# Optimization experiments

Hardware: AMD Instinct MI355X
Metric: run time of the kernel (lower is better)

Reference implementation:

```python
import jax, jax.numpy as jnp
import numpy as np

B, S, IN, H, T, OUT = 128, 336, 64, 1024, 96, 1


def _lstm_step(h, c, x, W_ih, W_hh, b_ih, b_hh):
    # PyTorch LSTM cell: gates in (i, f, g, o) order
    g = x @ W_ih.T + b_ih + h @ W_hh.T + b_hh  # [B, 4H]
    i, f, gg, o = jnp.split(g, 4, axis=-1)
    c_new = jax.nn.sigmoid(f) * c + jax.nn.sigmoid(i) * jnp.tanh(gg)
    h_new = jax.nn.sigmoid(o) * jnp.tanh(c_new)
    return h_new, c_new


def setup_inputs() -> dict:
    key = jax.random.key(0)
    ks = jax.random.split(key, 12)
    s = 0.05
    return {
        "src": jax.random.normal(ks[0], (B, S, IN), jnp.float32),
        "enc_W_ih": jax.random.normal(ks[1], (4 * H, IN), jnp.float32) * s,
        "enc_W_hh": jax.random.normal(ks[2], (4 * H, H), jnp.float32) * s,
        "enc_b_ih": jax.random.normal(ks[3], (4 * H,), jnp.float32) * s,
        "enc_b_hh": jax.random.normal(ks[4], (4 * H,), jnp.float32) * s,
        "dec_W_ih": jax.random.normal(ks[5], (4 * H, OUT + H), jnp.float32) * s,
        "dec_W_hh": jax.random.normal(ks[6], (4 * H, H), jnp.float32) * s,
        "dec_b_ih": jax.random.normal(ks[7], (4 * H,), jnp.float32) * s,
        "dec_b_hh": jax.random.normal(ks[8], (4 * H,), jnp.float32) * s,
        "attn_W": jax.random.normal(ks[9], (H, H), jnp.float32) * s,
        "fc_W": jax.random.normal(ks[10], (OUT, H), jnp.float32) * s,
        "fc_b": jax.random.normal(ks[11], (OUT,), jnp.float32) * s,
        "target_len": T,
    }


def reference(src, enc_W_ih, enc_W_hh, enc_b_ih, enc_b_hh,
              dec_W_ih, dec_W_hh, dec_b_ih, dec_b_hh,
              attn_W, fc_W, fc_b, target_len):
    batch = src.shape[0]
    hdim = enc_W_hh.shape[1]

    # ---- Encoder: single-layer LSTM over src, batch_first ----
    def enc_step(carry, x_t):
        h, c = carry
        h, c = _lstm_step(h, c, x_t, enc_W_ih, enc_W_hh, enc_b_ih, enc_b_hh)
        return (h, c), h

    h0 = jnp.zeros((batch, hdim), src.dtype)
    c0 = jnp.zeros((batch, hdim), src.dtype)
    (h_enc, c_enc), enc_hs = jax.lax.scan(enc_step, (h0, c0),
                                          jnp.swapaxes(src, 0, 1))
    encoder_outputs = jnp.swapaxes(enc_hs, 0, 1)  # [B, S, H]

    def dec_step(carry, _):
        h, c, prev_y = carry
        q = h @ attn_W.T                                      # [B, H]
        energy = jnp.einsum('bh,bsh->bs', q, encoder_outputs)  # [B, S]
        w = jax.nn.softmax(energy, axis=-1)
        ctx = jnp.einsum('bs,bsh->bh', w, encoder_outputs)     # [B, H]
        x = jnp.concatenate([prev_y, ctx], axis=-1)            # [B, OUT+H]
        h, c = _lstm_step(h, c, x, dec_W_ih, dec_W_hh, dec_b_ih, dec_b_hh)
        pred = h @ fc_W.T + fc_b                               # [B, OUT]
        prev_y = jax.lax.stop_gradient(pred)                   # pred.detach()
        return (h, c, prev_y), pred

    prev_y0 = jnp.zeros((batch, fc_W.shape[0]), src.dtype)
    _, preds = jax.lax.scan(dec_step, (h_enc, c_enc, prev_y0), None,
                            length=target_len)
    return jnp.swapaxes(preds, 0, 1)  # [B, target_len, OUT]
```

## Files before the change

### kernel.cpp

```cpp
#include <hip/hip_runtime.h>
#include <math.h>

#define Bn   128
#define Sn   336
#define INd  64
#define Hn   1024
#define Tn   96
#define G4   4096
#define KCE  34
#define KCD  65
#define KCQ  32
#define NBLK 256
#define SHALF 168

typedef __attribute__((ext_vector_type(8))) short short8;
typedef __attribute__((ext_vector_type(4))) float floatx4;
typedef __attribute__((ext_vector_type(4))) unsigned int uintx4;
typedef unsigned long long u64t;

__device__ __forceinline__ float sigmoidf_(float x){ return 1.0f/(1.0f+expf(-x)); }

__device__ __forceinline__ unsigned short f2bf(float f){
    union { float f; unsigned u; } v; v.f = f;
    unsigned r = v.u + 0x7fffu + ((v.u >> 16) & 1u);
    return (unsigned short)(r >> 16);
}
__device__ __forceinline__ float bflo(unsigned u){ union{unsigned u; float f;} v; v.u = u << 16;        return v.f; }
__device__ __forceinline__ float bfhi(unsigned u){ union{unsigned u; float f;} v; v.u = u & 0xffff0000u; return v.f; }
__device__ __forceinline__ void unpack8v(uintx4 v, float* f){
    f[0]=bflo(v.x); f[1]=bfhi(v.x); f[2]=bflo(v.y); f[3]=bfhi(v.y);
    f[4]=bflo(v.z); f[5]=bfhi(v.z); f[6]=bflo(v.w); f[7]=bfhi(v.w);
}

union Frag16 { u64t q[2]; short8 s8; uintx4 u4; };
union F2 { u64t q; float f[2]; };

__device__ __forceinline__ short8 ld_cg_s8(const unsigned short* p){
    Frag16 r;
    r.q[0] = __hip_atomic_load((const u64t*)p,     __ATOMIC_RELAXED, __HIP_MEMORY_SCOPE_AGENT);
    r.q[1] = __hip_atomic_load((const u64t*)p + 1, __ATOMIC_RELAXED, __HIP_MEMORY_SCOPE_AGENT);
    return r.s8;
}
__device__ __forceinline__ uintx4 ld_cg_u4(const unsigned short* p){
    Frag16 r;
    r.q[0] = __hip_atomic_load((const u64t*)p,     __ATOMIC_RELAXED, __HIP_MEMORY_SCOPE_AGENT);
    r.q[1] = __hip_atomic_load((const u64t*)p + 1, __ATOMIC_RELAXED, __HIP_MEMORY_SCOPE_AGENT);
    return r.u4;
}
__device__ __forceinline__ void st_cg16(unsigned short* p, unsigned short v){
    asm volatile("global_store_short %0, %1, off sc0 sc1" :: "v"(p), "v"((unsigned)v) : "memory");
}
__device__ __forceinline__ void st_cg32(unsigned short* p, unsigned v){
    asm volatile("global_store_dword %0, %1, off sc0 sc1" :: "v"(p), "v"(v) : "memory");
}
__device__ __forceinline__ void st_cg64(float* p, float a, float b){
    F2 v; v.f[0] = a; v.f[1] = b;
    __hip_atomic_store((u64t*)p, v.q, __ATOMIC_RELAXED, __HIP_MEMORY_SCOPE_AGENT);
}
__device__ __forceinline__ F2 ld_cg64(const float* p){
    F2 v; v.q = __hip_atomic_load((const u64t*)p, __ATOMIC_RELAXED, __HIP_MEMORY_SCOPE_AGENT);
    return v;
}

__device__ __forceinline__ void gbar3(unsigned* bb, unsigned step){
    asm volatile("s_waitcnt vmcnt(0)" ::: "memory");
    __syncthreads();
    if (threadIdx.x == 0)
        __hip_atomic_store(bb + blockIdx.x*32, step, __ATOMIC_RELAXED, __HIP_MEMORY_SCOPE_AGENT);
    if (blockIdx.x == 0){
        if (threadIdx.x < 64){
            const int l = threadIdx.x;
            for (;;){
                unsigned a0 = __hip_atomic_load(bb + (l      )*32, __ATOMIC_RELAXED, __HIP_MEMORY_SCOPE_AGENT);
                unsigned a1 = __hip_atomic_load(bb + (l +  64)*32, __ATOMIC_RELAXED, __HIP_MEMORY_SCOPE_AGENT);
                unsigned a2 = __hip_atomic_load(bb + (l + 128)*32, __ATOMIC_RELAXED, __HIP_MEMORY_SCOPE_AGENT);
                unsigned a3 = __hip_atomic_load(bb + (l + 192)*32, __ATOMIC_RELAXED, __HIP_MEMORY_SCOPE_AGENT);
                int ok = (a0 >= step) && (a1 >= step) && (a2 >= step) && (a3 >= step);
                if (__all(ok)) break;
                __builtin_amdgcn_s_sleep(1);
            }
            if (l == 0)
                __hip_atomic_store(bb + 8192, step, __ATOMIC_RELAXED, __HIP_MEMORY_SCOPE_AGENT);
        }
    } else {
        if (threadIdx.x == 0){
            while (__hip_atomic_load(bb + 8192, __ATOMIC_RELAXED, __HIP_MEMORY_SCOPE_AGENT) < step)
                __builtin_amdgcn_s_sleep(1);
        }
    }
    __syncthreads();
}

__global__ void pack_encf(const float* __restrict__ Wih, const float* __restrict__ Whh,
                          const float* __restrict__ bih, const float* __restrict__ bhh,
                          unsigned short* __restrict__ Wp, float* __restrict__ bc){
    long n = (long)256*KCE*512;
    for (long idx = (long)blockIdx.x*256 + threadIdx.x; idx < n; idx += (long)gridDim.x*256){
        int j = (int)(idx & 7), l = (int)((idx >> 3) & 63);
        int kc = (int)((idx >> 9) % KCE);
        int s  = (int)(idx / (KCE*512));
        int c = l & 15, kg = l >> 4;
        int k = kc*32 + kg*8 + j;
        int gate = s & 3, unit = (s >> 2)*16 + c;
        int orig = gate*Hn + unit;
        float v = (k < INd) ? Wih[orig*INd + k] : Whh[(size_t)orig*Hn + (k - INd)];
        Wp[idx] = f2bf(v);
    }
    int tid = blockIdx.x*256 + threadIdx.x;
    if (tid < G4){
        int g = (tid >> 4) & 3, u = (tid >> 6)*16 + (tid & 15);
        int orig = g*Hn + u;
        bc[tid] = bih[orig] + bhh[orig];
    }
}

__global__ void pack_decf(const float* __restrict__ Wih, const float* __restrict__ Whh,
                          const float* __restrict__ bih, const float* __restrict__ bhh,
                          unsigned short* __restrict__ Wp, float* __restrict__ bc){
    long n = (long)256*KCD*512;
    for (long idx = (long)blockIdx.x*256 + threadIdx.x; idx < n; idx += (long)gridDim.x*256){
        int j = (int)(idx & 7), l = (int)((idx >> 3) & 63);
        int kc = (int)((idx >> 9) % KCD);
        int s  = (int)(idx / (KCD*512));
        int c = l & 15, kg = l >> 4;
        int k = kc*32 + kg*8 + j;
        int gate = s & 3, unit = (s >> 2)*16 + c;
        int orig = gate*Hn + unit;
        float v;
        if (k < Hn)          v = Wih[(size_t)orig*(Hn+1) + 1 + k];
        else if (k < 2*Hn)   v = Whh[(size_t)orig*Hn + (k - Hn)];
        else if (k == 2*Hn)  v = Wih[(size_t)orig*(Hn+1)];
        else                 v = 0.0f;
        Wp[idx] = f2bf(v);
    }
    int tid = blockIdx.x*256 + threadIdx.x;
    if (tid < G4){
        int g = (tid >> 4) & 3, u = (tid >> 6)*16 + (tid & 15);
        int orig = g*Hn + u;
        bc[tid] = bih[orig] + bhh[orig];
    }
}

__global__ void pack_attnf(const float* __restrict__ w, unsigned short* __restrict__ Wp){
    int n = 64*KCQ*512;
    for (int idx = blockIdx.x*256 + threadIdx.x; idx < n; idx += gridDim.x*256){
        int j = idx & 7, l = (idx >> 3) & 63;
        int kc = (idx >> 9) & 31;
        int s  = idx >> 14;
        int nn = s*16 + (l & 15);
        int k = kc*32 + (l >> 4)*8 + j;
        Wp[idx] = f2bf(w[(size_t)nn*Hn + k]);
    }
}

__global__ void conv_srcf(const float* __restrict__ s, unsigned short* __restrict__ d){
    int n = Sn*8*2*512;
    for (int idx = blockIdx.x*256 + threadIdx.x; idx < n; idx += gridDim.x*256){
        int j = idx & 7, l = (idx >> 3) & 63;
        int kc = (idx >> 9) & 1, rg = (idx >> 10) & 7, t = idx >> 13;
        int b = rg*16 + (l & 15);
        int k = kc*32 + (l >> 4)*8 + j;
        d[idx] = f2bf(s[((size_t)b*Sn + t)*INd + k]);
    }
}

__global__ void init_ws(unsigned short* __restrict__ hf0, float* __restrict__ cbuf,
                        unsigned short* __restrict__ A0, unsigned short* __restrict__ A1,
                        unsigned* __restrict__ bars, unsigned* __restrict__ pcnt){
    int t0 = blockIdx.x*256 + threadIdx.x;
    for (int i = t0; i < 8*KCD*512; i += gridDim.x*256){
        A0[i] = 0; A1[i] = 0;
        if (i < 8*32*512) hf0[i] = 0;
        if (i < Bn*Hn) cbuf[i] = 0.0f;
        if (i < 32768) bars[i] = 0;
        if (i < 4096)  pcnt[i] = 0;
    }
}

__device__ __forceinline__ void swz(int b, int& x, int& y){
    int xcd = b & 7, li = b >> 3;
    y = xcd*8 + (li & 7);
    x = li >> 3;
}

__device__ __forceinline__ float fcdot(const unsigned short* __restrict__ hplain,
                                       const float* __restrict__ fcW, int b, int l){
    const unsigned short* hp = hplain + (size_t)b*Hn + l*16;
    uintx4 h0 = ld_cg_u4(hp), h1 = ld_cg_u4(hp + 8);
    float hf[16]; unpack8v(h0, hf); unpack8v(h1, hf + 8);
    float p = 0.0f;
    #pragma unroll
    for (int i = 0; i < 16; i++) p = fmaf(hf[i], fcW[l*16 + i], p);
    #pragma unroll
    for (int off = 32; off; off >>= 1) p += __shfl_down(p, off);
    return p;
}

__global__ __launch_bounds__(256, 1)
void enc_loop(const unsigned short* __restrict__ srcfrag,
              const unsigned short* __restrict__ Wf,
              const float* __restrict__ bc, float* __restrict__ cbuf,
              unsigned short* __restrict__ hf0,
              unsigned short* __restrict__ hf1,
              unsigned short* __restrict__ enco,
              unsigned short* __restrict__ adec0,
              unsigned* __restrict__ bar)
{
    __shared__ float red[2][16][65];
    const int tid = threadIdx.x, l = tid & 63, w = tid >> 6;
    const int rgw = w & 1, kh = w >> 1;
    int x, y; swz(blockIdx.x, x, y);
    const int rg = x*2 + rgw;
    const int m0 = rg*16;
    const unsigned short* Bf = Wf + (size_t)(4*y)*KCE*512 + l*8;

    const int col = l & 15, q = l >> 4;
    const int u = y*16 + col;
    const float bi  = bc[y*64 + col];
    const float bf_ = bc[y*64 + 16 + col];
    const float bg  = bc[y*64 + 32 + col];
    const float bo  = bc[y*64 + 48 + col];
    const int lsh = ((u >> 3) & 3) * 16;

    unsigned bstep = 0;
    for (int t = 0; t < Sn; t++){
        const unsigned short* hin = (t & 1) ? hf1 : hf0;
        unsigned short* hout      = (t & 1) ? hf0 : hf1;
        const unsigned short* Ah = hin + (size_t)rg*32*512 + l*8;
        floatx4 acc0={0,0,0,0}, acc1={0,0,0,0}, acc2={0,0,0,0}, acc3={0,0,0,0};

        if (kh == 0){
            short8 ah[15];
            #pragma unroll
            for (int hc = 0; hc < 15; hc++) ah[hc] = ld_cg_s8(Ah + hc*512);
            const unsigned short* Ax = srcfrag + ((size_t)t*8 + rg)*2*512 + l*8;
            #pragma unroll
            for (int kc = 0; kc < 2; kc++){
                short8 a  = *(const short8*)(Ax + kc*512);
                short8 b0 = *(const short8*)(Bf + (0*KCE + kc)*512);
                short8 b1 = *(const short8*)(Bf + (1*KCE + kc)*512);
                short8 b2 = *(const short8*)(Bf + (2*KCE + kc)*512);
                short8 b3 = *(const short8*)(Bf + (3*KCE + kc)*512);
                acc0 = __builtin_amdgcn_mfma_f32_16x16x32_bf16(a, b0, acc0, 0, 0, 0);
                acc1 = __builtin_amdgcn_mfma_f32_16x16x32_bf16(a, b1, acc1, 0, 0, 0);
                acc2 = __builtin_amdgcn_mfma_f32_16x16x32_bf16(a, b2, acc2, 0, 0, 0);
                acc3 = __builtin_amdgcn_mfma_f32_16x16x32_bf16(a, b3, acc3, 0, 0, 0);
            }
            #pragma unroll
            for (int hc = 0; hc < 15; hc++){
                short8 b0 = *(const short8*)(Bf + (0*KCE + hc + 2)*512);
                short8 b1 = *(const short8*)(Bf + (1*KCE + hc + 2)*512);
                short8 b2 = *(const short8*)(Bf + (2*KCE + hc + 2)*512);
                short8 b3 = *(const short8*)(Bf + (3*KCE + hc + 2)*512);
                acc0 = __builtin_amdgcn_mfma_f32_16x16x32_bf16(ah[hc], b0, acc0, 0, 0, 0);
                acc1 = __builtin_amdgcn_mfma_f32_16x16x32_bf16(ah[hc], b1, acc1, 0, 0, 0);
                acc2 = __builtin_amdgcn_mfma_f32_16x16x32_bf16(ah[hc], b2, acc2, 0, 0, 0);
                acc3 = __builtin_amdgcn_mfma_f32_16x16x32_bf16(ah[hc], b3, acc3, 0, 0, 0);
            }
        } else {
            short8 ah[17];
            #pragma unroll
            for (int i = 0; i < 17; i++) ah[i] = ld_cg_s8(Ah + (15 + i)*512);
            #pragma unroll
            for (int i = 0; i < 17; i++){
                short8 b0 = *(const short8*)(Bf + (0*KCE + i + 17)*512);
                short8 b1 = *(const short8*)(Bf + (1*KCE + i + 17)*512);
                short8 b2 = *(const short8*)(Bf + (2*KCE + i + 17)*512);
                short8 b3 = *(const short8*)(Bf + (3*KCE + i + 17)*512);
                acc0 = __builtin_amdgcn_mfma_f32_16x16x32_bf16(ah[i], b0, acc0, 0, 0, 0);
                acc1 = __builtin_amdgcn_mfma_f32_16x16x32_bf16(ah[i], b1, acc1, 0, 0, 0);
                acc2 = __builtin_amdgcn_mfma_f32_16x16x32_bf16(ah[i], b2, acc2, 0, 0, 0);
                acc3 = __builtin_amdgcn_mfma_f32_16x16x32_bf16(ah[i], b3, acc3, 0, 0, 0);
            }
            #pragma unroll
            for (int r = 0; r < 4; r++){
                red[rgw][ 0 + r][l] = acc0[r];
                red[rgw][ 4 + r][l] = acc1[r];
                red[rgw][ 8 + r][l] = acc2[r];
                red[rgw][12 + r][l] = acc3[r];
            }
        }
        __syncthreads();
        if (kh == 0){
            #pragma unroll
            for (int r = 0; r < 4; r++){
                acc0[r] += red[rgw][ 0 + r][l];
                acc1[r] += red[rgw][ 4 + r][l];
                acc2[r] += red[rgw][ 8 + r][l];
                acc3[r] += red[rgw][12 + r][l];
            }
            #pragma unroll
            for (int r = 0; r < 4; r++){
                const int m = m0 + q*4 + r;
                float gi = acc0[r] + bi;
                float gf = acc1[r] + bf_;
                float gg = acc2[r] + bg;
                float go = acc3[r] + bo;
                float co = cbuf[(size_t)m*Hn + u];
                float cn = sigmoidf_(gf)*co + sigmoidf_(gi)*tanhf(gg);
                float hv = sigmoidf_(go)*tanhf(cn);
                cbuf[(size_t)m*Hn + u] = cn;
                unsigned short hb = f2bf(hv);
                const int lanep = (q*4 + r) + lsh;
                st_cg16(hout + (((size_t)rg*32 + (u >> 5))*64 + lanep)*8 + (u & 7), hb);
                enco[((size_t)m*Sn + t)*Hn + u] = hb;
                if (t == Sn-1) adec0[(((size_t)rg*KCD + 32 + (u >> 5))*64 + lanep)*8 + (u & 7)] = hb;
            }
        }
        bstep++; gbar3(bar, bstep);
    }
}

#define BLOAD(P, I) { const size_t s_ = (size_t)(sb + 8*(I)); \
    buf_a##P = ebase[s_*128]; buf_b##P = ebase[s_*128 + 1]; }
#define BPROC(P) { \
    float ev[16]; unpack8v(buf_a##P, ev); unpack8v(buf_b##P, ev + 8); \
    float pt = 0.0f; \
    _Pragma("unroll") for (int i_ = 0; i_ < 16; i_++) pt = fmaf(qv[i_], ev[i_], pt); \
    _Pragma("unroll") for (int o_ = 32; o_; o_ >>= 1) pt += __shfl_down(pt, o_); \
    float e_ = __shfl(pt, 0); \
    float mn_ = fmaxf(mx, e_); \
    float corr_ = expf(mx - mn_); \
    float p_ = expf(e_ - mn_); \
    lsum = lsum*corr_ + p_; \
    if (corr_ != 1.0f){ _Pragma("unroll") for (int i_ = 0; i_ < 16; i_++) cacc[i_] *= corr_; } \
    _Pragma("unroll") for (int i_ = 0; i_ < 16; i_++) cacc[i_] = fmaf(p_, ev[i_], cacc[i_]); \
    mx = mn_; }

__global__ __launch_bounds__(512, 1)
void dec_loop(unsigned short* __restrict__ A0, unsigned short* __restrict__ A1,
              const unsigned short* __restrict__ Wdec,
              const float* __restrict__ bdec, float* __restrict__ cbuf,
              const unsigned short* __restrict__ Watt,
              unsigned short* __restrict__ qbf,
              const unsigned short* __restrict__ enco,
              unsigned short* __restrict__ hplain,
              float* __restrict__ pctx,
              float* __restrict__ pml,
              unsigned* __restrict__ pcnt,
              const float* __restrict__ fcW, const float* __restrict__ fcb,
              float* __restrict__ out, unsigned* __restrict__ bar)
{
    __shared__ float smem[8224];
    __shared__ unsigned cflag_s;
    const int tid = threadIdx.x, l = tid & 63, w = tid >> 6;
    const int rgw = w & 1, ks = w >> 1;
    int x, y; swz(blockIdx.x, x, y);
    const int rg = x*2 + rgw, m0 = rg*16;
    const unsigned short* Bf = Wdec + (size_t)(4*y)*KCD*512 + l*8;
    const unsigned short* Bq = Watt + (size_t)y*KCQ*512 + l*8;

    const int col = l & 15, q4 = l >> 4;
    const int u = y*16 + col;
    const float bi  = bdec[y*64 + col];
    const float bf_ = bdec[y*64 + 16 + col];
    const float bg  = bdec[y*64 + 32 + col];
    const float bo  = bdec[y*64 + 48 + col];
    const int lsh = ((u >> 3) & 3) * 16;
    const int ab   = blockIdx.x & 127;
    const int part = blockIdx.x >> 7;

    unsigned bstep = 0;
    for (int d = 0; d < Tn; d++){
        unsigned short* Ac = (d & 1) ? A1 : A0;
        unsigned short* An = (d & 1) ? A0 : A1;
        const unsigned short* Af = Ac + (size_t)rg*KCD*512 + l*8;

        floatx4 acc0={0,0,0,0}, acc1={0,0,0,0}, acc2={0,0,0,0}, acc3={0,0,0,0};
        {
            short8 aA[8];
            #pragma unroll
            for (int kk = 0; kk < 8; kk++)
                aA[kk] = ld_cg_s8(Af + (32 + ks*8 + kk)*512);
            floatx4 qa = {0,0,0,0};
            #pragma unroll
            for (int kk = 0; kk < 8; kk++){
                const int kc = 32 + ks*8 + kk;
                short8 b0 = *(const short8*)(Bf + (0*KCD + kc)*512);
                short8 b1 = *(const short8*)(Bf + (1*KCD + kc)*512);
                short8 b2 = *(const short8*)(Bf + (2*KCD + kc)*512);
                short8 b3 = *(const short8*)(Bf + (3*KCD + kc)*512);
                short8 bq = *(const short8*)(Bq + (ks*8 + kk)*512);
                acc0 = __builtin_amdgcn_mfma_f32_16x16x32_bf16(aA[kk], b0, acc0, 0, 0, 0);
                acc1 = __builtin_amdgcn_mfma_f32_16x16x32_bf16(aA[kk], b1, acc1, 0, 0, 0);
                acc2 = __builtin_amdgcn_mfma_f32_16x16x32_bf16(aA[kk], b2, acc2, 0, 0, 0);
                acc3 = __builtin_amdgcn_mfma_f32_16x16x32_bf16(aA[kk], b3, acc3, 0, 0, 0);
                qa   = __builtin_amdgcn_mfma_f32_16x16x32_bf16(aA[kk], bq, qa, 0, 0, 0);
            }
            #pragma unroll
            for (int r = 0; r < 4; r++) smem[(w*4 + r)*64 + l] = qa[r];
        }
        __syncthreads();
        if (ks == 0){
            #pragma unroll
            for (int r = 0; r < 4; r++){
                float s = smem[((0*2+rgw)*4 + r)*64 + l] + smem[((1*2+rgw)*4 + r)*64 + l]
                        + smem[((2*2+rgw)*4 + r)*64 + l] + smem[((3*2+rgw)*4 + r)*64 + l];
                st_cg16(qbf + (size_t)(m0 + q4*4 + r)*Hn + y*16 + col, f2bf(s));
            }
        }
        if (d > 0 && x == 0 && w >= 6){
            const int b = y*2 + (w & 1);
            float p = fcdot(hplain, fcW, b, l);
            if (l == 0){
                float pv = p + fcb[0];
                out[b*Tn + (d-1)] = pv;
                st_cg16(Ac + (((size_t)(b >> 4))*KCD + 64)*512 + (b & 15)*8, f2bf(pv));
            }
        }
        bstep++; gbar3(bar, bstep);

        {
            float* ctxl = smem;
            float* mred = smem + 8192;
            float* lred = smem + 8200;
            float qv[16];
            {
                const unsigned short* qp = qbf + (size_t)ab*Hn + l*16;
                uintx4 q0 = ld_cg_u4(qp), q1 = ld_cg_u4(qp + 8);
                unpack8v(q0, qv); unpack8v(q1, qv + 8);
            }
            float mx = -1e30f, lsum = 0.0f;
            float cacc[16];
            #pragma unroll
            for (int i = 0; i < 16; i++) cacc[i] = 0.0f;

            const uintx4* ebase = (const uintx4*)(enco + (size_t)ab*Sn*Hn) + l*2;
            const int sb = part*SHALF + w;
            uintx4 buf_a0, buf_b0, buf_a1, buf_b1, buf_a2, buf_b2, buf_a3, buf_b3;
            BLOAD(0,0)  BLOAD(1,1)  BLOAD(2,2)  BLOAD(3,3)
            BPROC(0) BLOAD(0,4)  BPROC(1) BLOAD(1,5)  BPROC(2) BLOAD(2,6)  BPROC(3) BLOAD(3,7)
            BPROC(0) BLOAD(0,8)  BPROC(1) BLOAD(1,9)  BPROC(2) BLOAD(2,10) BPROC(3) BLOAD(3,11)
            BPROC(0) BLOAD(0,12) BPROC(1) BLOAD(1,13) BPROC(2) BLOAD(2,14) BPROC(3) BLOAD(3,15)
            BPROC(0) BLOAD(0,16) BPROC(1) BLOAD(1,17) BPROC(2) BLOAD(2,18) BPROC(3) BLOAD(3,19)
            BPROC(0) BLOAD(0,20) BPROC(1) BPROC(2) BPROC(3)
            BPROC(0)

            if (l == 0){ mred[w] = mx; lred[w] = lsum; }
            __syncthreads();
            float M = mred[0];
            #pragma unroll
            for (int k = 1; k < 8; k++) M = fmaxf(M, mred[k]);
            float corr2 = expf(mx - M);
            #pragma unroll
            for (int j = 0; j < 16; j++) ctxl[w*1024 + j*64 + l] = cacc[j]*corr2;
            __syncthreads();
            float L = 0.0f;
            #pragma unroll
            for (int k = 0; k < 8; k++) L += lred[k]*expf(mred[k] - M);

            const int u0 = 2*tid;
            float s0 = 0.0f, s1 = 0.0f;
            #pragma unroll
            for (int k = 0; k < 8; k++){
                s0 += ctxl[k*1024 + (u0 & 15)*64 + (u0 >> 4)];
                s1 += ctxl[k*1024 + ((u0+1) & 15)*64 + ((u0+1) >> 4)];
            }
            st_cg64(pctx + ((size_t)part*128 + ab)*1024 + u0, s0, s1);
            if (tid == 0) st_cg64(pml + ((size_t)part*128 + ab)*2, M, lsum*0.0f + L);

            asm volatile("s_waitcnt vmcnt(0)" ::: "memory");
            __syncthreads();
            if (tid == 0){
                unsigned old = __hip_atomic_fetch_add(pcnt + ab*32, 1u,
                                  __ATOMIC_RELAXED, __HIP_MEMORY_SCOPE_AGENT);
                cflag_s = (old == 2u*(unsigned)d + 1u);
            }
            __syncthreads();
            if (cflag_s){
                F2 ml0 = ld_cg64(pml + (size_t)ab*2);
                F2 ml1 = ld_cg64(pml + (size_t)(128 + ab)*2);
                float Mg = fmaxf(ml0.f[0], ml1.f[0]);
                float w0 = expf(ml0.f[0] - Mg), w1 = expf(ml1.f[0] - Mg);
                float invL = 1.0f / (ml0.f[1]*w0 + ml1.f[1]*w1);
                F2 c0 = ld_cg64(pctx + (size_t)ab*1024 + u0);
                F2 c1 = ld_cg64(pctx + ((size_t)128 + ab)*1024 + u0);
                float v0 = (c0.f[0]*w0 + c1.f[0]*w1)*invL;
                float v1 = (c0.f[1]*w0 + c1.f[1]*w1)*invL;
                unsigned cvu = (unsigned)f2bf(v0) | ((unsigned)f2bf(v1) << 16);
                const int kcw = u0 >> 5;
                const int lanep2 = (ab & 15) + ((u0 >> 3) & 3)*16;
                st_cg32(Ac + ((((size_t)(ab >> 4))*KCD + kcw)*64 + lanep2)*8 + (u0 & 7), cvu);
            }
        }
        bstep++; gbar3(bar, bstep);

        {
            short8 aC[8];
            #pragma unroll
            for (int kk = 0; kk < 8; kk++)
                aC[kk] = ld_cg_s8(Af + (ks*8 + kk)*512);
            #pragma unroll
            for (int kk = 0; kk < 8; kk++){
                const int kc = ks*8 + kk;
                short8 b0 = *(const short8*)(Bf + (0*KCD + kc)*512);
                short8 b1 = *(const short8*)(Bf + (1*KCD + kc)*512);
                short8 b2 = *(const short8*)(Bf + (2*KCD + kc)*512);
                short8 b3 = *(const short8*)(Bf + (3*KCD + kc)*512);
                acc0 = __builtin_amdgcn_mfma_f32_16x16x32_bf16(aC[kk], b0, acc0, 0, 0, 0);
                acc1 = __builtin_amdgcn_mfma_f32_16x16x32_bf16(aC[kk], b1, acc1, 0, 0, 0);
                acc2 = __builtin_amdgcn_mfma_f32_16x16x32_bf16(aC[kk], b2, acc2, 0, 0, 0);
                acc3 = __builtin_amdgcn_mfma_f32_16x16x32_bf16(aC[kk], b3, acc3, 0, 0, 0);
            }
            if (ks == 3){
                short8 a  = ld_cg_s8(Af + 64*512);
                short8 b0 = *(const short8*)(Bf + (0*KCD + 64)*512);
                short8 b1 = *(const short8*)(Bf + (1*KCD + 64)*512);
                short8 b2 = *(const short8*)(Bf + (2*KCD + 64)*512);
                short8 b3 = *(const short8*)(Bf + (3*KCD + 64)*512);
                acc0 = __builtin_amdgcn_mfma_f32_16x16x32_bf16(a, b0, acc0, 0, 0, 0);
                acc1 = __builtin_amdgcn_mfma_f32_16x16x32_bf16(a, b1, acc1, 0, 0, 0);
                acc2 = __builtin_amdgcn_mfma_f32_16x16x32_bf16(a, b2, acc2, 0, 0, 0);
                acc3 = __builtin_amdgcn_mfma_f32_16x16x32_bf16(a, b3, acc3, 0, 0, 0);
            }
        }
        if (ks != 0){
            float* rp = smem + ((ks-1)*2 + rgw)*1024;
            #pragma unroll
            for (int r = 0; r < 4; r++){
                rp[( 0 + r)*64 + l] = acc0[r];
                rp[( 4 + r)*64 + l] = acc1[r];
                rp[( 8 + r)*64 + l] = acc2[r];
                rp[(12 + r)*64 + l] = acc3[r];
            }
        }
        __syncthreads();
        if (ks == 0){
            const float* r0 = smem + rgw*1024;
            const float* r1 = smem + (2 + rgw)*1024;
            const float* r2 = smem + (4 + rgw)*1024;
            #pragma unroll
            for (int r = 0; r < 4; r++){
                acc0[r] += r0[( 0+r)*64 + l] + r1[( 0+r)*64 + l] + r2[( 0+r)*64 + l];
                acc1[r] += r0[( 4+r)*64 + l] + r1[( 4+r)*64 + l] + r2[( 4+r)*64 + l];
                acc2[r] += r0[( 8+r)*64 + l] + r1[( 8+r)*64 + l] + r2[( 8+r)*64 + l];
                acc3[r] += r0[(12+r)*64 + l] + r1[(12+r)*64 + l] + r2[(12+r)*64 + l];
            }
            #pragma unroll
            for (int r = 0; r < 4; r++){
                const int m = m0 + q4*4 + r;
                float gi = acc0[r] + bi;
                float gf = acc1[r] + bf_;
                float gg = acc2[r] + bg;
                float go = acc3[r] + bo;
                float co = cbuf[(size_t)m*Hn + u];
                float cn = sigmoidf_(gf)*co + sigmoidf_(gi)*tanhf(gg);
                float hv = sigmoidf_(go)*tanhf(cn);
                cbuf[(size_t)m*Hn + u] = cn;
                unsigned short hb = f2bf(hv);
                const int lanep = (q4*4 + r) + lsh;
                st_cg16(An + (((size_t)rg*KCD + 32 + (u >> 5))*64 + lanep)*8 + (u & 7), hb);
                st_cg16(hplain + (size_t)m*Hn + u, hb);
            }
        }
        bstep++; gbar3(bar, bstep);
    }

    if (x == 0 && w >= 6){
        const int b = y*2 + (w & 1);
        float p = fcdot(hplain, fcW, b, l);
        if (l == 0) out[b*Tn + (Tn - 1)] = p + fcb[0];
    }
}

extern "C" void kernel_launch(void* const* d_in, const int* in_sizes, int n_in,
                              void* d_out, int out_size, void* d_ws, size_t ws_size,
                              hipStream_t stream){
    const float* src  = (const float*)d_in[0];
    const float* eWih = (const float*)d_in[1];
    const float* eWhh = (const float*)d_in[2];
    const float* ebih = (const float*)d_in[3];
    const float* ebhh = (const float*)d_in[4];
    const float* dWih = (const float*)d_in[5];
    const float* dWhh = (const float*)d_in[6];
    const float* dbih = (const float*)d_in[7];
    const float* dbhh = (const float*)d_in[8];
    const float* attnW= (const float*)d_in[9];
    const float* fcW  = (const float*)d_in[10];
    const float* fcb  = (const float*)d_in[11];
    float* out = (float*)d_out;

    char* base = (char*)d_ws;
    auto alloc = [&](size_t bytes){ void* p = base; base += (bytes + 255) & ~255ull; return p; };
    unsigned short* Wencf = (unsigned short*)alloc((size_t)256*KCE*512*2);
    float*          benc  = (float*)alloc(G4*4);
    unsigned short* Wdecf = (unsigned short*)alloc((size_t)256*KCD*512*2);
    float*          bdec  = (float*)alloc(G4*4);
    unsigned short* Wattf = (unsigned short*)alloc((size_t)64*KCQ*512*2);
    unsigned short* srcf  = (unsigned short*)alloc((size_t)Sn*8*2*512*2);
    unsigned short* enco  = (unsigned short*)alloc((size_t)Bn*Sn*Hn*2);
    unsigned short* hf0   = (unsigned short*)alloc((size_t)8*32*512*2);
    unsigned short* hf1   = (unsigned short*)alloc((size_t)8*32*512*2);
    float*          cbuf  = (float*)alloc((size_t)Bn*Hn*4);
    unsigned short* A0f   = (unsigned short*)alloc((size_t)8*KCD*512*2);
    unsigned short* A1f   = (unsigned short*)alloc((size_t)8*KCD*512*2);
    unsigned short* qbf   = (unsigned short*)alloc((size_t)Bn*Hn*2);
    unsigned short* hplain= (unsigned short*)alloc((size_t)Bn*Hn*2);
    float*          pctx  = (float*)alloc((size_t)2*128*1024*4);
    float*          pml   = (float*)alloc((size_t)2*128*2*4);
    unsigned*       bars  = (unsigned*)alloc((size_t)32768*4);
    unsigned*       pcnt  = (unsigned*)alloc((size_t)4096*4);

    conv_srcf<<<2048, 256, 0, stream>>>(src, srcf);
    pack_encf<<<4096, 256, 0, stream>>>(eWih, eWhh, ebih, ebhh, Wencf, benc);
    pack_decf<<<8192, 256, 0, stream>>>(dWih, dWhh, dbih, dbhh, Wdecf, bdec);
    pack_attnf<<<1024, 256, 0, stream>>>(attnW, Wattf);
    init_ws<<<1040, 256, 0, stream>>>(hf0, cbuf, A0f, A1f, bars, pcnt);

    enc_loop<<<NBLK, 256, 0, stream>>>(srcf, Wencf, benc, cbuf, hf0, hf1,
                                       enco, A0f, bars);
    dec_loop<<<NBLK, 512, 0, stream>>>(A0f, A1f, Wdecf, bdec, cbuf, Wattf,
                                       qbf, enco, hplain, pctx, pml, pcnt,
                                       fcW, fcb, out, bars + 16384);
}
```

Measured before the change: 10.87 ms.

## Use group-local barriers in encoder, per-block release flags, and 1024-thread decoder

The encoder's grid-wide barrier becomes a per-row-group barrier, since each group of 64 blocks sharing an x index only depends on its own h rows. The full barrier now writes a per-block release flag so waiters do not all poll one address, and the sleep interval grows. The decoder moves from 512 to 1024 threads, so 16 waves split the attention scan over the sequence, while the MFMA phases still use the original 8 waves. This trades a larger block and more idle waves during the GEMM phases for more memory parallelism in attention and less barrier contention.

```diff
diff --git a/kernel.cpp b/kernel.cpp
--- a/kernel.cpp
+++ b/kernel.cpp
@@ -62,7 +62,7 @@
     return v;
 }
 
-__device__ __forceinline__ void gbar3(unsigned* bb, unsigned step){
+__device__ __forceinline__ void gbar_full(unsigned* bb, unsigned step){
     asm volatile("s_waitcnt vmcnt(0)" ::: "memory");
     __syncthreads();
     if (threadIdx.x == 0)
@@ -71,21 +71,50 @@
         if (threadIdx.x < 64){
             const int l = threadIdx.x;
             for (;;){
-                unsigned a0 = __hip_atomic_load(bb + (l      )*32, __ATOMIC_RELAXED, __HIP_MEMORY_SCOPE_AGENT);
-                unsigned a1 = __hip_atomic_load(bb + (l +  64)*32, __ATOMIC_RELAXED, __HIP_MEMORY_SCOPE_AGENT);
-                unsigned a2 = __hip_atomic_load(bb + (l + 128)*32, __ATOMIC_RELAXED, __HIP_MEMORY_SCOPE_AGENT);
-                unsigned a3 = __hip_atomic_load(bb + (l + 192)*32, __ATOMIC_RELAXED, __HIP_MEMORY_SCOPE_AGENT);
-                int ok = (a0 >= step) && (a1 >= step) && (a2 >= step) && (a3 >= step);
+                int ok = 1;
+                #pragma unroll
+                for (int i = 0; i < 4; i++){
+                    unsigned a = __hip_atomic_load(bb + (l + i*64)*32,
+                                    __ATOMIC_RELAXED, __HIP_MEMORY_SCOPE_AGENT);
+                    ok &= (a >= step);
+                }
                 if (__all(ok)) break;
-                __builtin_amdgcn_s_sleep(1);
-            }
-            if (l == 0)
-                __hip_atomic_store(bb + 8192, step, __ATOMIC_RELAXED, __HIP_MEMORY_SCOPE_AGENT);
+                __builtin_amdgcn_s_sleep(2);
+            }
+            #pragma unroll
+            for (int i = 0; i < 4; i++)
+                __hip_atomic_store(bb + 8192 + (l + i*64)*32, step,
+                                   __ATOMIC_RELAXED, __HIP_MEMORY_SCOPE_AGENT);
         }
     } else {
         if (threadIdx.x == 0){
-            while (__hip_atomic_load(bb + 8192, __ATOMIC_RELAXED, __HIP_MEMORY_SCOPE_AGENT) < step)
-                __builtin_amdgcn_s_sleep(1);
+            while (__hip_atomic_load(bb + 8192 + blockIdx.x*32,
+                      __ATOMIC_RELAXED, __HIP_MEMORY_SCOPE_AGENT) < step)
+                __builtin_amdgcn_s_sleep(2);
+        }
+    }
+    __syncthreads();
+}
+
+__device__ __forceinline__ void gbar_grp(unsigned* gb, int gi, unsigned step){
+    asm volatile("s_waitcnt vmcnt(0)" ::: "memory");
+    __syncthreads();
+    if (threadIdx.x == 0)
+        __hip_atomic_store(gb + gi*32, step, __ATOMIC_RELAXED, __HIP_MEMORY_SCOPE_AGENT);
+    if (gi == 0){
+        if (threadIdx.x < 64){
+            const int l = threadIdx.x;
+            while (__hip_atomic_load(gb + l*32, __ATOMIC_RELAXED,
+                                     __HIP_MEMORY_SCOPE_AGENT) < step)
+                __builtin_amdgcn_s_sleep(2);
+            __hip_atomic_store(gb + 4096 + l*32, step,
+                               __ATOMIC_RELAXED, __HIP_MEMORY_SCOPE_AGENT);
+        }
+    } else {
+        if (threadIdx.x == 0){
+            while (__hip_atomic_load(gb + 4096 + gi*32, __ATOMIC_RELAXED,
+                                     __HIP_MEMORY_SCOPE_AGENT) < step)
+                __builtin_amdgcn_s_sleep(2);
         }
     }
     __syncthreads();
@@ -172,7 +201,7 @@
         A0[i] = 0; A1[i] = 0;
         if (i < 8*32*512) hf0[i] = 0;
         if (i < Bn*Hn) cbuf[i] = 0.0f;
-        if (i < 32768) bars[i] = 0;
+        if (i < 49152) bars[i] = 0;
         if (i < 4096)  pcnt[i] = 0;
     }
 }
@@ -210,6 +239,8 @@
     const int tid = threadIdx.x, l = tid & 63, w = tid >> 6;
     const int rgw = w & 1, kh = w >> 1;
     int x, y; swz(blockIdx.x, x, y);
+    unsigned* gb = bar + x*8192;
+    const int gi = y;
     const int rg = x*2 + rgw;
     const int m0 = rg*16;
     const unsigned short* Bf = Wf + (size_t)(4*y)*KCE*512 + l*8;
@@ -292,12 +323,12 @@
             #pragma unroll
             for (int r = 0; r < 4; r++){
                 const int m = m0 + q*4 + r;
-                float gi = acc0[r] + bi;
+                float gi_ = acc0[r] + bi;
                 float gf = acc1[r] + bf_;
                 float gg = acc2[r] + bg;
                 float go = acc3[r] + bo;
                 float co = cbuf[(size_t)m*Hn + u];
-                float cn = sigmoidf_(gf)*co + sigmoidf_(gi)*tanhf(gg);
+                float cn = sigmoidf_(gf)*co + sigmoidf_(gi_)*tanhf(gg);
                 float hv = sigmoidf_(go)*tanhf(cn);
                 cbuf[(size_t)m*Hn + u] = cn;
                 unsigned short hb = f2bf(hv);
@@ -307,27 +338,11 @@
                 if (t == Sn-1) adec0[(((size_t)rg*KCD + 32 + (u >> 5))*64 + lanep)*8 + (u & 7)] = hb;
             }
         }
-        bstep++; gbar3(bar, bstep);
-    }
-}
-
-#define BLOAD(P, I) { const size_t s_ = (size_t)(sb + 8*(I)); \
-    buf_a##P = ebase[s_*128]; buf_b##P = ebase[s_*128 + 1]; }
-#define BPROC(P) { \
-    float ev[16]; unpack8v(buf_a##P, ev); unpack8v(buf_b##P, ev + 8); \
-    float pt = 0.0f; \
-    _Pragma("unroll") for (int i_ = 0; i_ < 16; i_++) pt = fmaf(qv[i_], ev[i_], pt); \
-    _Pragma("unroll") for (int o_ = 32; o_; o_ >>= 1) pt += __shfl_down(pt, o_); \
-    float e_ = __shfl(pt, 0); \
-    float mn_ = fmaxf(mx, e_); \
-    float corr_ = expf(mx - mn_); \
-    float p_ = expf(e_ - mn_); \
-    lsum = lsum*corr_ + p_; \
-    if (corr_ != 1.0f){ _Pragma("unroll") for (int i_ = 0; i_ < 16; i_++) cacc[i_] *= corr_; } \
-    _Pragma("unroll") for (int i_ = 0; i_ < 16; i_++) cacc[i_] = fmaf(p_, ev[i_], cacc[i_]); \
-    mx = mn_; }
-
-__global__ __launch_bounds__(512, 1)
+        bstep++; gbar_grp(gb, gi, bstep);
+    }
+}
+
+__global__ __launch_bounds__(1024, 4)
 void dec_loop(unsigned short* __restrict__ A0, unsigned short* __restrict__ A1,
               const unsigned short* __restrict__ Wdec,
               const float* __restrict__ bdec, float* __restrict__ cbuf,
@@ -367,7 +382,7 @@
         const unsigned short* Af = Ac + (size_t)rg*KCD*512 + l*8;
 
         floatx4 acc0={0,0,0,0}, acc1={0,0,0,0}, acc2={0,0,0,0}, acc3={0,0,0,0};
-        {
+        if (w < 8){
             short8 aA[8];
             #pragma unroll
             for (int kk = 0; kk < 8; kk++)
@@ -390,16 +405,7 @@
             #pragma unroll
             for (int r = 0; r < 4; r++) smem[(w*4 + r)*64 + l] = qa[r];
         }
-        __syncthreads();
-        if (ks == 0){
-            #pragma unroll
-            for (int r = 0; r < 4; r++){
-                float s = smem[((0*2+rgw)*4 + r)*64 + l] + smem[((1*2+rgw)*4 + r)*64 + l]
-                        + smem[((2*2+rgw)*4 + r)*64 + l] + smem[((3*2+rgw)*4 + r)*64 + l];
-                st_cg16(qbf + (size_t)(m0 + q4*4 + r)*Hn + y*16 + col, f2bf(s));
-            }
-        }
-        if (d > 0 && x == 0 && w >= 6){
+        if (d > 0 && x == 0 && w >= 14){
             const int b = y*2 + (w & 1);
             float p = fcdot(hplain, fcW, b, l);
             if (l == 0){
@@ -408,12 +414,21 @@
                 st_cg16(Ac + (((size_t)(b >> 4))*KCD + 64)*512 + (b & 15)*8, f2bf(pv));
             }
         }
-        bstep++; gbar3(bar, bstep);
+        __syncthreads();
+        if (w < 8 && ks == 0){
+            #pragma unroll
+            for (int r = 0; r < 4; r++){
+                float s = smem[((0*2+rgw)*4 + r)*64 + l] + smem[((1*2+rgw)*4 + r)*64 + l]
+                        + smem[((2*2+rgw)*4 + r)*64 + l] + smem[((3*2+rgw)*4 + r)*64 + l];
+                st_cg16(qbf + (size_t)(m0 + q4*4 + r)*Hn + y*16 + col, f2bf(s));
+            }
+        }
+        bstep++; gbar_full(bar, bstep);
 
         {
             float* ctxl = smem;
             float* mred = smem + 8192;
-            float* lred = smem + 8200;
+            float* lred = smem + 8208;
             float qv[16];
             {
                 const unsigned short* qp = qbf + (size_t)ab*Hn + l*16;
@@ -426,38 +441,61 @@
             for (int i = 0; i < 16; i++) cacc[i] = 0.0f;
 
             const uintx4* ebase = (const uintx4*)(enco + (size_t)ab*Sn*Hn) + l*2;
-            const int sb = part*SHALF + w;
-            uintx4 buf_a0, buf_b0, buf_a1, buf_b1, buf_a2, buf_b2, buf_a3, buf_b3;
-            BLOAD(0,0)  BLOAD(1,1)  BLOAD(2,2)  BLOAD(3,3)
-            BPROC(0) BLOAD(0,4)  BPROC(1) BLOAD(1,5)  BPROC(2) BLOAD(2,6)  BPROC(3) BLOAD(3,7)
-            BPROC(0) BLOAD(0,8)  BPROC(1) BLOAD(1,9)  BPROC(2) BLOAD(2,10) BPROC(3) BLOAD(3,11)
-            BPROC(0) BLOAD(0,12) BPROC(1) BLOAD(1,13) BPROC(2) BLOAD(2,14) BPROC(3) BLOAD(3,15)
-            BPROC(0) BLOAD(0,16) BPROC(1) BLOAD(1,17) BPROC(2) BLOAD(2,18) BPROC(3) BLOAD(3,19)
-            BPROC(0) BLOAD(0,20) BPROC(1) BPROC(2) BPROC(3)
-            BPROC(0)
-
+            const int s0i = part*SHALF;
+            for (int s = s0i + w; s < s0i + SHALF; s += 16){
+                uintx4 e0 = ebase[(size_t)s*128];
+                uintx4 e1 = ebase[(size_t)s*128 + 1];
+                float ev[16];
+                unpack8v(e0, ev); unpack8v(e1, ev + 8);
+                float pt = 0.0f;
+                #pragma unroll
+                for (int i = 0; i < 16; i++) pt = fmaf(qv[i], ev[i], pt);
+                #pragma unroll
+                for (int off = 32; off; off >>= 1) pt += __shfl_down(pt, off);
+                float e = __shfl(pt, 0);
+                float mn = fmaxf(mx, e);
+                float corr = expf(mx - mn);
+                float p = expf(e - mn);
+                lsum = lsum*corr + p;
+                if (corr != 1.0f){
+                    #pragma unroll
+                    for (int i = 0; i < 16; i++) cacc[i] *= corr;
+                }
+                #pragma unroll
+                for (int i = 0; i < 16; i++) cacc[i] = fmaf(p, ev[i], cacc[i]);
+                mx = mn;
+            }
             if (l == 0){ mred[w] = mx; lred[w] = lsum; }
             __syncthreads();
             float M = mred[0];
             #pragma unroll
-            for (int k = 1; k < 8; k++) M = fmaxf(M, mred[k]);
+            for (int k = 1; k < 16; k++) M = fmaxf(M, mred[k]);
             float corr2 = expf(mx - M);
-            #pragma unroll
-            for (int j = 0; j < 16; j++) ctxl[w*1024 + j*64 + l] = cacc[j]*corr2;
+            if (w < 8){
+                #pragma unroll
+                for (int j = 0; j < 16; j++) ctxl[w*1024 + j*64 + l] = cacc[j]*corr2;
+            }
+            __syncthreads();
+            if (w >= 8){
+                #pragma unroll
+                for (int j = 0; j < 16; j++) ctxl[(w-8)*1024 + j*64 + l] += cacc[j]*corr2;
+            }
             __syncthreads();
             float L = 0.0f;
             #pragma unroll
-            for (int k = 0; k < 8; k++) L += lred[k]*expf(mred[k] - M);
-
-            const int u0 = 2*tid;
-            float s0 = 0.0f, s1 = 0.0f;
-            #pragma unroll
-            for (int k = 0; k < 8; k++){
-                s0 += ctxl[k*1024 + (u0 & 15)*64 + (u0 >> 4)];
-                s1 += ctxl[k*1024 + ((u0+1) & 15)*64 + ((u0+1) >> 4)];
-            }
-            st_cg64(pctx + ((size_t)part*128 + ab)*1024 + u0, s0, s1);
-            if (tid == 0) st_cg64(pml + ((size_t)part*128 + ab)*2, M, lsum*0.0f + L);
+            for (int k = 0; k < 16; k++) L += lred[k]*expf(mred[k] - M);
+
+            if (tid < 512){
+                const int u0 = 2*tid;
+                float s0 = 0.0f, s1 = 0.0f;
+                #pragma unroll
+                for (int k = 0; k < 8; k++){
+                    s0 += ctxl[k*1024 + (u0 & 15)*64 + (u0 >> 4)];
+                    s1 += ctxl[k*1024 + ((u0+1) & 15)*64 + ((u0+1) >> 4)];
+                }
+                st_cg64(pctx + ((size_t)part*128 + ab)*1024 + u0, s0, s1);
+            }
+            if (tid == 0) st_cg64(pml + ((size_t)part*128 + ab)*2, M, L);
 
             asm volatile("s_waitcnt vmcnt(0)" ::: "memory");
             __syncthreads();
@@ -467,7 +505,8 @@
                 cflag_s = (old == 2u*(unsigned)d + 1u);
             }
             __syncthreads();
-            if (cflag_s){
+            if (cflag_s && tid < 512){
+                const int u0 = 2*tid;
                 F2 ml0 = ld_cg64(pml + (size_t)ab*2);
                 F2 ml1 = ld_cg64(pml + (size_t)(128 + ab)*2);
                 float Mg = fmaxf(ml0.f[0], ml1.f[0]);
@@ -483,9 +522,9 @@
                 st_cg32(Ac + ((((size_t)(ab >> 4))*KCD + kcw)*64 + lanep2)*8 + (u0 & 7), cvu);
             }
         }
-        bstep++; gbar3(bar, bstep);
-
-        {
+        bstep++; gbar_full(bar, bstep);
+
+        if (w < 8){
             short8 aC[8];
             #pragma unroll
             for (int kk = 0; kk < 8; kk++)
@@ -513,19 +552,19 @@
                 acc2 = __builtin_amdgcn_mfma_f32_16x16x32_bf16(a, b2, acc2, 0, 0, 0);
                 acc3 = __builtin_amdgcn_mfma_f32_16x16x32_bf16(a, b3, acc3, 0, 0, 0);
             }
-        }
-        if (ks != 0){
-            float* rp = smem + ((ks-1)*2 + rgw)*1024;
-            #pragma unroll
-            for (int r = 0; r < 4; r++){
-                rp[( 0 + r)*64 + l] = acc0[r];
-                rp[( 4 + r)*64 + l] = acc1[r];
-                rp[( 8 + r)*64 + l] = acc2[r];
-                rp[(12 + r)*64 + l] = acc3[r];
+            if (ks != 0){
+                float* rp = smem + ((ks-1)*2 + rgw)*1024;
+                #pragma unroll
+                for (int r = 0; r < 4; r++){
+                    rp[( 0 + r)*64 + l] = acc0[r];
+                    rp[( 4 + r)*64 + l] = acc1[r];
+                    rp[( 8 + r)*64 + l] = acc2[r];
+                    rp[(12 + r)*64 + l] = acc3[r];
+                }
             }
         }
         __syncthreads();
-        if (ks == 0){
+        if (w < 8 && ks == 0){
             const float* r0 = smem + rgw*1024;
             const float* r1 = smem + (2 + rgw)*1024;
             const float* r2 = smem + (4 + rgw)*1024;
@@ -553,10 +592,10 @@
                 st_cg16(hplain + (size_t)m*Hn + u, hb);
             }
         }
-        bstep++; gbar3(bar, bstep);
-    }
-
-    if (x == 0 && w >= 6){
+        bstep++; gbar_full(bar, bstep);
+    }
+
+    if (x == 0 && w >= 14){
         const int b = y*2 + (w & 1);
         float p = fcdot(hplain, fcW, b, l);
         if (l == 0) out[b*Tn + (Tn - 1)] = p + fcb[0];
@@ -598,7 +637,7 @@
     unsigned short* hplain= (unsigned short*)alloc((size_t)Bn*Hn*2);
     float*          pctx  = (float*)alloc((size_t)2*128*1024*4);
     float*          pml   = (float*)alloc((size_t)2*128*2*4);
-    unsigned*       bars  = (unsigned*)alloc((size_t)32768*4);
+    unsigned*       bars  = (unsigned*)alloc((size_t)49152*4);
     unsigned*       pcnt  = (unsigned*)alloc((size_t)4096*4);
 
     conv_srcf<<<2048, 256, 0, stream>>>(src, srcf);
@@ -609,7 +648,7 @@
 
     enc_loop<<<NBLK, 256, 0, stream>>>(srcf, Wencf, benc, cbuf, hf0, hf1,
                                        enco, A0f, bars);
-    dec_loop<<<NBLK, 512, 0, stream>>>(A0f, A1f, Wdecf, bdec, cbuf, Wattf,
-                                       qbf, enco, hplain, pctx, pml, pcnt,
-                                       fcW, fcb, out, bars + 16384);
-}
+    dec_loop<<<NBLK, 1024, 0, stream>>>(A0f, A1f, Wdecf, bdec, cbuf, Wattf,
+                                        qbf, enco, hplain, pctx, pml, pcnt,
+                                        fcW, fcb, out, bars + 32768);
+}
```

After: 11.31 ms. +4.0%, slower.
